# Performance work log

Hardware: AMD Instinct MI355X
Metric: run time of the kernel (lower is better)

## Reference

```python
import jax, jax.numpy as jnp
import numpy as np

B, S, D, H = 2, 2048, 1024, 16
DK = D // H


def setup_inputs() -> dict:
    key = jax.random.key(0)
    ks = jax.random.split(key, 8)
    query = jax.random.normal(ks[0], (B, S, D), dtype=jnp.float32)
    key_t = jax.random.normal(ks[1], (B, S, D), dtype=jnp.float32)
    value = jax.random.normal(ks[2], (B, S, D), dtype=jnp.float32)
    # causal mask (1 = attend, 0 = masked), broadcast over batch and heads
    mask = jnp.tril(jnp.ones((S, S), dtype=jnp.int32))[None, None, :, :]
    scale = 1.0 / np.sqrt(D)
    w_q = jax.random.normal(ks[3], (D, D), dtype=jnp.float32) * scale
    w_k = jax.random.normal(ks[4], (D, D), dtype=jnp.float32) * scale
    w_v = jax.random.normal(ks[5], (D, D), dtype=jnp.float32) * scale
    w_o = jax.random.normal(ks[6], (D, D), dtype=jnp.float32) * scale
    b_o = jnp.zeros((D,), dtype=jnp.float32)
    return {"query": query, "key": key_t, "value": value, "mask": mask,
            "w_q": w_q, "w_k": w_k, "w_v": w_v, "w_o": w_o, "b_o": b_o}


def reference(query, key, value, mask, w_q, w_k, w_v, w_o, b_o):
    # projections: nn.Linear applies x @ W.T; weights here stored as [out, in]
    def proj(x, w):  # [B,S,D] -> [B,H,S,DK]
        y = jnp.einsum('bsd,ed->bse', x, w)
        return y.reshape(B, S, H, DK).transpose(0, 2, 1, 3)

    Q = proj(query, w_q)
    K = proj(key, w_k)
    V = proj(value, w_v)

    scores = jnp.einsum('bhqd,bhkd->bhqk', Q, K) / jnp.sqrt(jnp.float32(DK))
    scores = jnp.where(mask == 0, jnp.float32(-1e9), scores)
    attention_weights = jax.nn.softmax(scores, axis=-1)  # dropout p=0 (eval)
    context = jnp.einsum('bhqk,bhkd->bhqd', attention_weights, V)
    context = context.transpose(0, 2, 1, 3).reshape(B, S, D)
    output = jnp.einsum('bsd,ed->bse', context, w_o) + b_o
    return output, attention_weights
```

## Files before the change

kernel.cpp:

```cpp
#include <hip/hip_runtime.h>
#include <hip/hip_bf16.h>
#include <math.h>

#define B_  2
#define S_  2048
#define D_  1024
#define H_  16
#define DK_ 64

typedef __attribute__((ext_vector_type(8))) short bf16x8;
typedef __attribute__((ext_vector_type(4))) float f32x4;
typedef __attribute__((ext_vector_type(8))) unsigned short u16x8;
typedef __attribute__((ext_vector_type(4))) unsigned short u16x4;

#define MFMA16(a, b, c) __builtin_amdgcn_mfma_f32_16x16x32_bf16((a), (b), (c), 0, 0, 0)

__device__ __forceinline__ unsigned short f2bf(float f) {
    union { float f; unsigned u; } v; v.f = f;
    unsigned r = v.u + 0x7fffu + ((v.u >> 16) & 1u);
    return (unsigned short)(r >> 16);
}
__device__ __forceinline__ float bf2f(unsigned short u) {
    return __uint_as_float(((unsigned)u) << 16);
}

__device__ __forceinline__ void gload16(const unsigned short* g, unsigned short* l) {
    __builtin_amdgcn_global_load_lds(
        (const __attribute__((address_space(1))) unsigned int*)g,
        (__attribute__((address_space(3))) unsigned int*)l, 16, 0, 0);
}

__global__ __launch_bounds__(256) void cvt_all(
        const float* __restrict__ q, const float* __restrict__ k, const float* __restrict__ v,
        const float* __restrict__ wq, const float* __restrict__ wk,
        const float* __restrict__ wv, const float* __restrict__ wo,
        unsigned short* __restrict__ xq, unsigned short* __restrict__ xk,
        unsigned short* __restrict__ xv, unsigned short* __restrict__ wqb,
        unsigned short* __restrict__ wkb, unsigned short* __restrict__ wvb,
        unsigned short* __restrict__ wob) {
    int i = blockIdx.x * 256 + threadIdx.x;
    const float* src; unsigned short* dst; int off;
    if      (i < 1048576) { src = q;  dst = xq;  off = 0; }
    else if (i < 2097152) { src = k;  dst = xk;  off = 1048576; }
    else if (i < 3145728) { src = v;  dst = xv;  off = 2097152; }
    else if (i < 3407872) { src = wq; dst = wqb; off = 3145728; }
    else if (i < 3670016) { src = wk; dst = wkb; off = 3407872; }
    else if (i < 3932160) { src = wv; dst = wvb; off = 3670016; }
    else                  { src = wo; dst = wob; off = 3932160; }
    i -= off;
    f32x4 f = __builtin_nontemporal_load(reinterpret_cast<const f32x4*>(src) + i);
    ushort4 o;
    o.x = f2bf(f[0]); o.y = f2bf(f[1]); o.z = f2bf(f[2]); o.w = f2bf(f[3]);
    reinterpret_cast<ushort4*>(dst)[i] = o;
}

__device__ __forceinline__ void gemm_bt_body(char* smem, int blk,
        const unsigned short* __restrict__ A, const unsigned short* __restrict__ W,
        void* __restrict__ out, const float* __restrict__ bias, int mode, float scale) {
    const int lane = threadIdx.x & 63;
    const int row  = lane & 15, quad = lane >> 4;
    const int w    = threadIdx.x >> 6;
    const int bmi  = blk & 31;
    const int bni  = blk >> 5;
    const int m0b  = bmi * 128, n0b = bni * 128;
    const int m0   = m0b + (w >> 1) * 64;
    const int n0   = n0b + (w & 1) * 64;

    unsigned short* Ab = (unsigned short*)smem;
    unsigned short* Wb = Ab + 4096;

    const int c0    = w * 2;
    const int srow  = c0 * 16 + (lane >> 2);
    const int scol  = (lane & 3) * 8;
    const unsigned short* gA0 = A + (size_t)(m0b + srow) * D_ + scol;
    const unsigned short* gA1 = gA0 + 16 * D_;
    const unsigned short* gW0 = W + (size_t)(n0b + srow) * D_ + scol;
    const unsigned short* gW1 = gW0 + 16 * D_;
    unsigned short* lA0 = Ab + c0 * 512;
    unsigned short* lA1 = lA0 + 512;
    unsigned short* lW0 = Wb + c0 * 512;
    unsigned short* lW1 = lW0 + 512;

    const int arow = (w >> 1) * 64 + row;
    const int wrow = (w & 1) * 64 + row;
    f32x4 acc[4][4] = {};
    for (int k0 = 0; k0 < D_; k0 += 32) {
        gload16(gA0 + k0, lA0);
        gload16(gA1 + k0, lA1);
        gload16(gW0 + k0, lW0);
        gload16(gW1 + k0, lW1);
        __syncthreads();
        bf16x8 a0 = *(const bf16x8*)(Ab + (arow     ) * 32 + quad * 8);
        bf16x8 a1 = *(const bf16x8*)(Ab + (arow + 16) * 32 + quad * 8);
        bf16x8 a2 = *(const bf16x8*)(Ab + (arow + 32) * 32 + quad * 8);
        bf16x8 a3 = *(const bf16x8*)(Ab + (arow + 48) * 32 + quad * 8);
        bf16x8 w0 = *(const bf16x8*)(Wb + (wrow     ) * 32 + quad * 8);
        bf16x8 w1 = *(const bf16x8*)(Wb + (wrow + 16) * 32 + quad * 8);
        bf16x8 w2 = *(const bf16x8*)(Wb + (wrow + 32) * 32 + quad * 8);
        bf16x8 w3 = *(const bf16x8*)(Wb + (wrow + 48) * 32 + quad * 8);
        acc[0][0] = MFMA16(a0, w0, acc[0][0]);
        acc[0][1] = MFMA16(a0, w1, acc[0][1]);
        acc[0][2] = MFMA16(a0, w2, acc[0][2]);
        acc[0][3] = MFMA16(a0, w3, acc[0][3]);
        acc[1][0] = MFMA16(a1, w0, acc[1][0]);
        acc[1][1] = MFMA16(a1, w1, acc[1][1]);
        acc[1][2] = MFMA16(a1, w2, acc[1][2]);
        acc[1][3] = MFMA16(a1, w3, acc[1][3]);
        acc[2][0] = MFMA16(a2, w0, acc[2][0]);
        acc[2][1] = MFMA16(a2, w1, acc[2][1]);
        acc[2][2] = MFMA16(a2, w2, acc[2][2]);
        acc[2][3] = MFMA16(a2, w3, acc[2][3]);
        acc[3][0] = MFMA16(a3, w0, acc[3][0]);
        acc[3][1] = MFMA16(a3, w1, acc[3][1]);
        acc[3][2] = MFMA16(a3, w2, acc[3][2]);
        acc[3][3] = MFMA16(a3, w3, acc[3][3]);
        __syncthreads();
    }

    char* myep = smem + w * 9216;
    const int b = m0 >> 11;
    const int h = n0 >> 6;
    if (mode == 0) {
        unsigned short* lt = (unsigned short*)myep;
#pragma unroll
        for (int mi = 0; mi < 4; mi++)
#pragma unroll
            for (int t = 0; t < 4; t++)
#pragma unroll
                for (int r = 0; r < 4; r++)
                    lt[(mi * 16 + quad * 4 + r) * 72 + t * 16 + row] = f2bf(acc[mi][t][r] * scale);
        __builtin_amdgcn_sched_barrier(0);
        unsigned short* Qout = (unsigned short*)out;
#pragma unroll
        for (int pass = 0; pass < 8; pass++) {
            int rr = pass * 8 + (lane >> 3);
            int cc = (lane & 7) * 8;
            u16x8 val = *(const u16x8*)(lt + rr * 72 + cc);
            int s = (m0 + rr) & (S_ - 1);
            *(u16x8*)(&Qout[(((size_t)(b * H_ + h)) * S_ + s) * DK_ + cc]) = val;
        }
    } else if (mode == 1) {
        unsigned short* lt = (unsigned short*)myep;
#pragma unroll
        for (int mi = 0; mi < 4; mi++)
#pragma unroll
            for (int t = 0; t < 4; t++)
#pragma unroll
                for (int r = 0; r < 4; r++)
                    lt[(t * 16 + row) * 72 + mi * 16 + quad * 4 + r] = f2bf(acc[mi][t][r]);
        __builtin_amdgcn_sched_barrier(0);
        unsigned short* Vout = (unsigned short*)out;
#pragma unroll
        for (int pass = 0; pass < 8; pass++) {
            int dk = pass * 8 + (lane >> 3);
            int so = (lane & 7) * 8;
            u16x8 val = *(const u16x8*)(lt + dk * 72 + so);
            *(u16x8*)(&Vout[(((size_t)(b * H_ + h)) * DK_ + dk) * S_ + (m0 & (S_ - 1)) + so]) = val;
        }
    } else {
        float* lt32 = (float*)myep;
        float bs[4];
#pragma unroll
        for (int t = 0; t < 4; t++) bs[t] = bias[n0 + t * 16 + row];
        float* outF = (float*)out;
#pragma unroll
        for (int mh = 0; mh < 2; mh++) {
#pragma unroll
            for (int mi2 = 0; mi2 < 2; mi2++)
#pragma unroll
                for (int t = 0; t < 4; t++)
#pragma unroll
                    for (int r = 0; r < 4; r++)
                        lt32[(mi2 * 16 + quad * 4 + r) * 72 + t * 16 + row] =
                            acc[mh * 2 + mi2][t][r] + bs[t];
            __builtin_amdgcn_sched_barrier(0);
#pragma unroll
            for (int pass = 0; pass < 8; pass++) {
                int rr = pass * 4 + (lane >> 4);
                int cc = (lane & 15) * 4;
                f32x4 val = *(const f32x4*)(lt32 + rr * 72 + cc);
                __builtin_nontemporal_store(val,
                    (f32x4*)(&outF[(size_t)(m0 + mh * 32 + rr) * D_ + n0 + cc]));
            }
            __builtin_amdgcn_sched_barrier(0);
        }
    }
}

__global__ __launch_bounds__(256) void gemm_qkv(
        const unsigned short* __restrict__ xq, const unsigned short* __restrict__ xk,
        const unsigned short* __restrict__ xv, const unsigned short* __restrict__ wqb,
        const unsigned short* __restrict__ wkb, const unsigned short* __restrict__ wvb,
        unsigned short* __restrict__ Qb, unsigned short* __restrict__ Kb,
        unsigned short* __restrict__ Vt) {
    __shared__ char smem[36864];
    const int which = blockIdx.x >> 8;
    const int blk   = blockIdx.x & 255;
    if (which == 0)      gemm_bt_body(smem, blk, xq, wqb, Qb, nullptr, 0, 0.125f);
    else if (which == 1) gemm_bt_body(smem, blk, xk, wkb, Kb, nullptr, 0, 1.0f);
    else                 gemm_bt_body(smem, blk, xv, wvb, Vt, nullptr, 1, 1.0f);
}

__global__ __launch_bounds__(256) void gemm_out(
        const unsigned short* __restrict__ A, const unsigned short* __restrict__ W,
        float* __restrict__ out, const float* __restrict__ bias) {
    __shared__ char smem[36864];
    gemm_bt_body(smem, blockIdx.x, A, W, out, bias, 2, 1.0f);
}

__global__ __launch_bounds__(256) void attn_kernel(const unsigned short* __restrict__ Qb,
                                                   const unsigned short* __restrict__ Kb,
                                                   const unsigned short* __restrict__ Vt,
                                                   float* __restrict__ Pbase,
                                                   unsigned short* __restrict__ ctx) {
    __shared__ unsigned short plds[4][16 * 40];
    __shared__ float olds[4][16 * 64];
    __shared__ float llds[4][16];
    const int w    = threadIdx.x >> 6;
    const int lane = threadIdx.x & 63;
    const int row  = lane & 15, quad = lane >> 4;
    const int tile = 127 - (int)(blockIdx.x >> 5);
    const int bh   = blockIdx.x & 31;
    const int q0   = tile * 16;
    const int b    = bh >> 4, h = bh & 15;
    const unsigned short* Qh = Qb + (size_t)bh * S_ * DK_;
    const unsigned short* Kh = Kb + (size_t)bh * S_ * DK_;
    const unsigned short* Vh = Vt + (size_t)bh * DK_ * S_;
    float* P = Pbase + (size_t)bh * S_ * S_;

    bf16x8 aq0 = *(const bf16x8*)(Qh + (q0 + row) * DK_ + quad * 8);
    bf16x8 aq1 = *(const bf16x8*)(Qh + (q0 + row) * DK_ + 32 + quad * 8);

    const int nks   = (q0 + 47) >> 5;
    const int nfull = (q0 + 1) >> 5;

    float l_l[4] = {0.f, 0.f, 0.f, 0.f};
    for (int ks = w; ks < nks; ks += 4) {
        const int c0k = ks * 32;
        const bool diag = (ks >= nfull);
#pragma unroll
        for (int half = 0; half < 2; half++) {
            const int c = c0k + half * 16;
            const unsigned short* kp = Kh + (c + row) * DK_ + quad * 8;
            bf16x8 k0 = *(const bf16x8*)kp;
            bf16x8 k1 = *(const bf16x8*)(kp + 32);
            f32x4 sa = {};
            sa = MFMA16(aq0, k0, sa);
            sa = MFMA16(aq1, k1, sa);
#pragma unroll
            for (int r = 0; r < 4; r++) {
                float p = __expf(sa[r]);
                if (diag) p = ((c + row) <= (q0 + quad * 4 + r)) ? p : 0.f;
                l_l[r] += p;
            }
        }
    }
#pragma unroll
    for (int r = 0; r < 4; r++) {
#pragma unroll
        for (int off = 1; off < 16; off <<= 1)
            l_l[r] += __shfl_xor(l_l[r], off, 16);
        if (row == 0) llds[w][quad * 4 + r] = l_l[r];
    }
    __syncthreads();
    float invL[4];
#pragma unroll
    for (int r = 0; r < 4; r++)
        invL[r] = 1.0f / (llds[0][quad * 4 + r] + llds[1][quad * 4 + r] +
                          llds[2][quad * 4 + r] + llds[3][quad * 4 + r]);

    f32x4 o[4] = {};
    unsigned short* myld = plds[w];
    for (int ks = w; ks < nks; ks += 4) {
        const int c0k = ks * 32;
        const bool diag = (ks >= nfull);
#pragma unroll
        for (int half = 0; half < 2; half++) {
            const int c = c0k + half * 16;
            const unsigned short* kp = Kh + (c + row) * DK_ + quad * 8;
            bf16x8 k0 = *(const bf16x8*)kp;
            bf16x8 k1 = *(const bf16x8*)(kp + 32);
            f32x4 sa = {};
            sa = MFMA16(aq0, k0, sa);
            sa = MFMA16(aq1, k1, sa);
#pragma unroll
            for (int r = 0; r < 4; r++) {
                float p = __expf(sa[r]) * invL[r];
                if (diag) p = ((c + row) <= (q0 + quad * 4 + r)) ? p : 0.f;
                myld[(quad * 4 + r) * 40 + half * 16 + row] = f2bf(p);
            }
        }
        __builtin_amdgcn_sched_barrier(0);
#pragma unroll
        for (int g = 0; g < 2; g++) {
            int rr = g * 8 + (lane >> 3);
            int cg = (lane & 7) * 4;
            u16x4 pb = *(const u16x4*)(myld + rr * 40 + cg);
            f32x4 pv;
            pv[0] = bf2f((unsigned short)pb[0]);
            pv[1] = bf2f((unsigned short)pb[1]);
            pv[2] = bf2f((unsigned short)pb[2]);
            pv[3] = bf2f((unsigned short)pb[3]);
            __builtin_nontemporal_store(pv, (f32x4*)(&P[(size_t)(q0 + rr) * S_ + c0k + cg]));
        }
        bf16x8 pf = *(const bf16x8*)(myld + row * 40 + quad * 8);
#pragma unroll
        for (int t4 = 0; t4 < 4; t4++) {
            bf16x8 vv = *(const bf16x8*)(Vh + (t4 * 16 + row) * S_ + c0k + quad * 8);
            o[t4] = MFMA16(pf, vv, o[t4]);
        }
        __builtin_amdgcn_sched_barrier(0);
    }

    float* myo = olds[w];
#pragma unroll
    for (int t4 = 0; t4 < 4; t4++)
#pragma unroll
        for (int r = 0; r < 4; r++)
            myo[(quad * 4 + r) * 64 + t4 * 16 + row] = o[t4][r];
    __syncthreads();
    {
        int i  = threadIdx.x;
        int rr = i >> 4, c4 = (i & 15) * 4;
        u16x4 cv;
#pragma unroll
        for (int j = 0; j < 4; j++) {
            float s = olds[0][rr * 64 + c4 + j] + olds[1][rr * 64 + c4 + j] +
                      olds[2][rr * 64 + c4 + j] + olds[3][rr * 64 + c4 + j];
            cv[j] = (short)f2bf(s);
        }
        *(u16x4*)(&ctx[((size_t)(b * S_) + q0 + rr) * D_ + h * DK_ + c4]) = cv;
    }

    const int cb = nks * 32;
    if (cb < S_) {
        const f32x4 z = {0.f, 0.f, 0.f, 0.f};
#pragma unroll 1
        for (int rr = 0; rr < 16; rr++) {
            float* Pr = &P[(size_t)(q0 + rr) * S_];
            for (int cc = cb + threadIdx.x * 4; cc < S_; cc += 1024)
                __builtin_nontemporal_store(z, reinterpret_cast<f32x4*>(Pr + cc));
        }
    }
}

extern "C" void kernel_launch(void* const* d_in, const int* in_sizes, int n_in,
                              void* d_out, int out_size, void* d_ws, size_t ws_size,
                              hipStream_t stream) {
    const float* q  = (const float*)d_in[0];
    const float* k  = (const float*)d_in[1];
    const float* v  = (const float*)d_in[2];
    const float* wq = (const float*)d_in[4];
    const float* wk = (const float*)d_in[5];
    const float* wv = (const float*)d_in[6];
    const float* wo = (const float*)d_in[7];
    const float* bo = (const float*)d_in[8];

    unsigned short* ws  = (unsigned short*)d_ws;
    unsigned short* xq  = ws;
    unsigned short* xk  = ws + 4194304;
    unsigned short* xv  = ws + 8388608;
    unsigned short* wqb = ws + 12582912;
    unsigned short* wkb = wqb + 1048576;
    unsigned short* wvb = wkb + 1048576;
    unsigned short* wob = wvb + 1048576;
    unsigned short* Qb  = ws + 16777216;
    unsigned short* Kb  = Qb + 4194304;
    unsigned short* Vt  = Kb + 4194304;
    unsigned short* ctx = Vt + 4194304;
    float* outp  = (float*)d_out;
    float* Pbase = outp + 4194304;

    cvt_all<<<16384, 256, 0, stream>>>(q, k, v, wq, wk, wv, wo,
                                       xq, xk, xv, wqb, wkb, wvb, wob);

    gemm_qkv<<<768, 256, 0, stream>>>(xq, xk, xv, wqb, wkb, wvb, Qb, Kb, Vt);

    attn_kernel<<<4096, 256, 0, stream>>>(Qb, Kb, Vt, Pbase, ctx);

    gemm_out<<<256, 256, 0, stream>>>(ctx, wob, outp, bo);
}
```

Measured before the change: 765.3 us.

## Stage full unnormalized P row-block in LDS to avoid recomputing QK^T

The attention kernel now computes QK^T and exp once, writes unnormalized bf16 probabilities for the whole 16-row block into a 64KB swizzled LDS buffer, and reduces row sums across 8 waves. It then splits the waves: four compute P·V from LDS per 16-column slice of the head dimension and normalize at the end, while the other four stream the normalized P rows and zero tail to global memory. This removes the second QK^T/exp pass and the cross-wave output reduction. In exchange it uses 64KB of LDS per block, which limits occupancy, and doubles the block size to 512 threads.

```diff
diff --git a/kernel.cpp b/kernel.cpp
--- a/kernel.cpp
+++ b/kernel.cpp
@@ -208,17 +208,16 @@
     gemm_bt_body(smem, blockIdx.x, A, W, out, bias, 2, 1.0f);
 }
 
-__global__ __launch_bounds__(256) void attn_kernel(const unsigned short* __restrict__ Qb,
+__global__ __launch_bounds__(512) void attn_kernel(const unsigned short* __restrict__ Qb,
                                                    const unsigned short* __restrict__ Kb,
                                                    const unsigned short* __restrict__ Vt,
                                                    float* __restrict__ Pbase,
                                                    unsigned short* __restrict__ ctx) {
-    __shared__ unsigned short plds[4][16 * 40];
-    __shared__ float olds[4][16 * 64];
-    __shared__ float llds[4][16];
+    __shared__ unsigned short Pt[16 * 2048];
+    __shared__ float llds[8][16];
     const int w    = threadIdx.x >> 6;
     const int lane = threadIdx.x & 63;
-    const int row  = lane & 15, quad = lane >> 4;
+    const int kidx = lane & 15, quad = lane >> 4;
     const int tile = 127 - (int)(blockIdx.x >> 5);
     const int bh   = blockIdx.x & 31;
     const int q0   = tile * 16;
@@ -227,21 +226,22 @@
     const unsigned short* Kh = Kb + (size_t)bh * S_ * DK_;
     const unsigned short* Vh = Vt + (size_t)bh * DK_ * S_;
     float* P = Pbase + (size_t)bh * S_ * S_;
-
-    bf16x8 aq0 = *(const bf16x8*)(Qh + (q0 + row) * DK_ + quad * 8);
-    bf16x8 aq1 = *(const bf16x8*)(Qh + (q0 + row) * DK_ + 32 + quad * 8);
+    char* Pc = (char*)Pt;
+
+    bf16x8 aq0 = *(const bf16x8*)(Qh + (q0 + kidx) * DK_ + quad * 8);
+    bf16x8 aq1 = *(const bf16x8*)(Qh + (q0 + kidx) * DK_ + 32 + quad * 8);
 
     const int nks   = (q0 + 47) >> 5;
     const int nfull = (q0 + 1) >> 5;
 
     float l_l[4] = {0.f, 0.f, 0.f, 0.f};
-    for (int ks = w; ks < nks; ks += 4) {
+    for (int ks = w; ks < nks; ks += 8) {
         const int c0k = ks * 32;
         const bool diag = (ks >= nfull);
 #pragma unroll
         for (int half = 0; half < 2; half++) {
             const int c = c0k + half * 16;
-            const unsigned short* kp = Kh + (c + row) * DK_ + quad * 8;
+            const unsigned short* kp = Kh + (c + kidx) * DK_ + quad * 8;
             bf16x8 k0 = *(const bf16x8*)kp;
             bf16x8 k1 = *(const bf16x8*)(kp + 32);
             f32x4 sa = {};
@@ -249,9 +249,13 @@
             sa = MFMA16(aq1, k1, sa);
 #pragma unroll
             for (int r = 0; r < 4; r++) {
+                const int qrow = quad * 4 + r;
                 float p = __expf(sa[r]);
-                if (diag) p = ((c + row) <= (q0 + quad * 4 + r)) ? p : 0.f;
+                if (diag) p = ((c + kidx) <= (q0 + qrow)) ? p : 0.f;
                 l_l[r] += p;
+                int byte = qrow * 4096 + (c + kidx) * 2;
+                byte ^= (qrow & 7) << 4;
+                *(unsigned short*)(Pc + byte) = f2bf(p);
             }
         }
     }
@@ -260,87 +264,53 @@
 #pragma unroll
         for (int off = 1; off < 16; off <<= 1)
             l_l[r] += __shfl_xor(l_l[r], off, 16);
-        if (row == 0) llds[w][quad * 4 + r] = l_l[r];
+        if (kidx == 0) llds[w][quad * 4 + r] = l_l[r];
     }
     __syncthreads();
-    float invL[4];
-#pragma unroll
-    for (int r = 0; r < 4; r++)
-        invL[r] = 1.0f / (llds[0][quad * 4 + r] + llds[1][quad * 4 + r] +
-                          llds[2][quad * 4 + r] + llds[3][quad * 4 + r]);
-
-    f32x4 o[4] = {};
-    unsigned short* myld = plds[w];
-    for (int ks = w; ks < nks; ks += 4) {
-        const int c0k = ks * 32;
-        const bool diag = (ks >= nfull);
-#pragma unroll
-        for (int half = 0; half < 2; half++) {
-            const int c = c0k + half * 16;
-            const unsigned short* kp = Kh + (c + row) * DK_ + quad * 8;
-            bf16x8 k0 = *(const bf16x8*)kp;
-            bf16x8 k1 = *(const bf16x8*)(kp + 32);
-            f32x4 sa = {};
-            sa = MFMA16(aq0, k0, sa);
-            sa = MFMA16(aq1, k1, sa);
-#pragma unroll
-            for (int r = 0; r < 4; r++) {
-                float p = __expf(sa[r]) * invL[r];
-                if (diag) p = ((c + row) <= (q0 + quad * 4 + r)) ? p : 0.f;
-                myld[(quad * 4 + r) * 40 + half * 16 + row] = f2bf(p);
-            }
-        }
-        __builtin_amdgcn_sched_barrier(0);
-#pragma unroll
-        for (int g = 0; g < 2; g++) {
-            int rr = g * 8 + (lane >> 3);
-            int cg = (lane & 7) * 4;
-            u16x4 pb = *(const u16x4*)(myld + rr * 40 + cg);
-            f32x4 pv;
-            pv[0] = bf2f((unsigned short)pb[0]);
-            pv[1] = bf2f((unsigned short)pb[1]);
-            pv[2] = bf2f((unsigned short)pb[2]);
-            pv[3] = bf2f((unsigned short)pb[3]);
-            __builtin_nontemporal_store(pv, (f32x4*)(&P[(size_t)(q0 + rr) * S_ + c0k + cg]));
-        }
-        bf16x8 pf = *(const bf16x8*)(myld + row * 40 + quad * 8);
-#pragma unroll
-        for (int t4 = 0; t4 < 4; t4++) {
-            bf16x8 vv = *(const bf16x8*)(Vh + (t4 * 16 + row) * S_ + c0k + quad * 8);
-            o[t4] = MFMA16(pf, vv, o[t4]);
-        }
-        __builtin_amdgcn_sched_barrier(0);
-    }
-
-    float* myo = olds[w];
-#pragma unroll
-    for (int t4 = 0; t4 < 4; t4++)
-#pragma unroll
-        for (int r = 0; r < 4; r++)
-            myo[(quad * 4 + r) * 64 + t4 * 16 + row] = o[t4][r];
-    __syncthreads();
-    {
-        int i  = threadIdx.x;
-        int rr = i >> 4, c4 = (i & 15) * 4;
-        u16x4 cv;
-#pragma unroll
-        for (int j = 0; j < 4; j++) {
-            float s = olds[0][rr * 64 + c4 + j] + olds[1][rr * 64 + c4 + j] +
-                      olds[2][rr * 64 + c4 + j] + olds[3][rr * 64 + c4 + j];
-            cv[j] = (short)f2bf(s);
-        }
-        *(u16x4*)(&ctx[((size_t)(b * S_) + q0 + rr) * D_ + h * DK_ + c4]) = cv;
-    }
-
-    const int cb = nks * 32;
-    if (cb < S_) {
+
+    if (w < 4) {
+        const unsigned short* Vd = Vh + (size_t)(w * 16 + kidx) * S_ + quad * 8;
+        f32x4 o = {};
+        const int mswz = (kidx & 7) << 4;
+        for (int ks = 0; ks < nks; ks++) {
+            int byteA = (kidx * 4096 + (ks * 32 + quad * 8) * 2) ^ mswz;
+            bf16x8 pf = *(const bf16x8*)(Pc + byteA);
+            bf16x8 vv = *(const bf16x8*)(Vd + ks * 32);
+            o = MFMA16(pf, vv, o);
+        }
+#pragma unroll
+        for (int r = 0; r < 4; r++) {
+            const int qrow = quad * 4 + r;
+            float inv = 1.0f / (llds[0][qrow] + llds[1][qrow] + llds[2][qrow] + llds[3][qrow] +
+                                llds[4][qrow] + llds[5][qrow] + llds[6][qrow] + llds[7][qrow]);
+            ctx[((size_t)(b * S_) + q0 + qrow) * D_ + h * DK_ + w * 16 + kidx] =
+                f2bf(o[r] * inv);
+        }
+    } else {
+        const int r0 = (w - 4) * 4 + quad;
+        float inv = 1.0f / (llds[0][r0] + llds[1][r0] + llds[2][r0] + llds[3][r0] +
+                            llds[4][r0] + llds[5][r0] + llds[6][r0] + llds[7][r0]);
+        const int cb = nks * 32;
+        float* Pr = &P[(size_t)(q0 + r0) * S_];
+        const char* Prow = Pc + r0 * 4096;
+        const int sw = (r0 & 7) << 4;
+        for (int c = (kidx) * 8; c < cb; c += 128) {
+            u16x8 pb = *(const u16x8*)(Prow + ((c * 2) ^ sw));
+            f32x4 lo, hi;
+            lo[0] = bf2f((unsigned short)pb[0]) * inv;
+            lo[1] = bf2f((unsigned short)pb[1]) * inv;
+            lo[2] = bf2f((unsigned short)pb[2]) * inv;
+            lo[3] = bf2f((unsigned short)pb[3]) * inv;
+            hi[0] = bf2f((unsigned short)pb[4]) * inv;
+            hi[1] = bf2f((unsigned short)pb[5]) * inv;
+            hi[2] = bf2f((unsigned short)pb[6]) * inv;
+            hi[3] = bf2f((unsigned short)pb[7]) * inv;
+            __builtin_nontemporal_store(lo, (f32x4*)(Pr + c));
+            __builtin_nontemporal_store(hi, (f32x4*)(Pr + c + 4));
+        }
         const f32x4 z = {0.f, 0.f, 0.f, 0.f};
-#pragma unroll 1
-        for (int rr = 0; rr < 16; rr++) {
-            float* Pr = &P[(size_t)(q0 + rr) * S_];
-            for (int cc = cb + threadIdx.x * 4; cc < S_; cc += 1024)
-                __builtin_nontemporal_store(z, reinterpret_cast<f32x4*>(Pr + cc));
-        }
+        for (int c = cb + kidx * 4; c < S_; c += 64)
+            __builtin_nontemporal_store(z, (f32x4*)(Pr + c));
     }
 }
 
@@ -376,7 +346,7 @@
 
     gemm_qkv<<<768, 256, 0, stream>>>(xq, xk, xv, wqb, wkb, wvb, Qb, Kb, Vt);
 
-    attn_kernel<<<4096, 256, 0, stream>>>(Qb, Kb, Vt, Pbase, ctx);
+    attn_kernel<<<4096, 512, 0, stream>>>(Qb, Kb, Vt, Pbase, ctx);
 
     gemm_out<<<256, 256, 0, stream>>>(ctx, wob, outp, bo);
 }
```

New measurement: 772.3 us. No clear change (+0.9%).
